# Optimization experiments

Hardware: AMD Instinct MI355X
Metric: run time of the kernel (lower is better)

Reference implementation:

```python
import jax, jax.numpy as jnp
import numpy as np

B, N, D, H = 64, 196, 768, 3072
QMAX = 127.0  # 8-bit symmetric: clamp to [-128, 127]


def ste_round(x):
    # straight-through-estimator round (QAT)
    return x + jax.lax.stop_gradient(jnp.round(x) - x)


def q_linear_diag(x, w, b, a_sf):
    """Quantized diagonal linear (ResMLP Affine / LayerScale as QuantLinear)."""
    w_sf = jnp.max(jnp.abs(w)) / QMAX            # per-tensor weight scale
    w_int = ste_round(w / w_sf)                  # int8 weights (|.|<=127)
    out_int = (x / a_sf) * w_int
    if b is not None:
        out_int = out_int + ste_round(b / (a_sf * w_sf))  # 32-bit bias
    return out_int * (a_sf * w_sf), w_sf


def q_linear_dense(x, w, b, a_sf):
    """Quantized dense linear: int8 GEMM + int32 bias, dequant with a_sf*w_sf."""
    w_sf = jnp.max(jnp.abs(w)) / QMAX
    w_int = jnp.clip(ste_round(w / w_sf), -QMAX - 1, QMAX)
    out_int = jnp.einsum('...i,oi->...o', x / a_sf, w_int) + ste_round(b / (a_sf * w_sf))
    return out_int * (a_sf * w_sf), w_sf


def q_act(x, pre_sf, new_sf, identity=None, id_sf=None):
    """HAWQ-style QuantAct: fixed-point requantization to scale new_sf (8-bit)."""
    if identity is None:
        z_int = ste_round(x / pre_sf)
        out_int = ste_round(z_int * (pre_sf / new_sf))
    else:
        # main branch (x - identity) requantized with pre_sf, identity with id_sf
        z_int = ste_round((x - identity) / pre_sf)
        out_int = ste_round(z_int * (pre_sf / new_sf)) \
                + ste_round(ste_round(identity / id_sf) * (id_sf / new_sf))
    out_int = jnp.clip(out_int, -QMAX - 1, QMAX)
    return out_int * new_sf, new_sf


def _forward(x, norm1_w, norm1_b, attn_w, attn_b, gamma1_w,
             norm2_w, norm2_b, fc1_w, fc1_b, fc2_w, fc2_b, gamma2_w, act_sfs):
    a_sf = act_sfs[0]
    # --- token-mixing half ---
    identity, id_sf = x, a_sf
    x, w_sf = q_linear_diag(x, norm1_w, norm1_b, a_sf)         # norm1 (affine)
    x = jnp.swapaxes(x, 1, 2)                                  # [B, D, N]
    x, a_sf = q_act(x, a_sf * w_sf, act_sfs[1])                # quant_act1
    x, w_sf = q_linear_dense(x, attn_w, attn_b, a_sf)          # attn (cross-patch)
    x = jnp.swapaxes(x, 1, 2)                                  # [B, N, D]
    x, a_sf = q_act(x, a_sf * w_sf, act_sfs[2])                # quant_act2
    x, w_sf = q_linear_diag(x, gamma1_w, None, a_sf)           # gamma_1 (layerscale)
    x = x + identity
    x, a_sf = q_act(x, a_sf * w_sf, act_sfs[3], identity, id_sf)  # quant_act_int32_1
    # --- MLP half ---
    identity, id_sf = x, a_sf
    x, w_sf = q_linear_diag(x, norm2_w, norm2_b, a_sf)         # norm2
    x, a_sf = q_act(x, a_sf * w_sf, act_sfs[4])                # quant_act3
    x, w_sf = q_linear_dense(x, fc1_w, fc1_b, a_sf)            # mlp.fc1
    x = jax.nn.relu(x)
    x, a_sf = q_act(x, a_sf * w_sf, act_sfs[5])                # mlp.quant_act1
    x, w_sf = q_linear_dense(x, fc2_w, fc2_b, a_sf)            # mlp.fc2
    x, a_sf = q_act(x, a_sf * w_sf, act_sfs[6])                # mlp.quant_act2
    x, w_sf = q_linear_diag(x, gamma2_w, None, a_sf)           # gamma_2
    x = x + identity
    x, a_sf = q_act(x, a_sf * w_sf, act_sfs[7], identity, id_sf)  # quant_act_int32_2
    return x, a_sf


def setup_inputs() -> dict:
    key = jax.random.key(0)
    ks = jax.random.split(key, 16)
    act_sfs = jax.random.uniform(ks[14], (8,), jnp.float32, 0.02, 0.06)
    x = jax.random.normal(ks[0], (B, N, D), jnp.float32)
    # input is already quantized at scale act_sfs[0]
    x = jnp.clip(jnp.round(x / act_sfs[0]), -128, 127) * act_sfs[0]
    s = 0.05
    return {
        'x': x,
        'norm1_w': 1.0 + s * jax.random.normal(ks[1], (D,), jnp.float32),
        'norm1_b': s * jax.random.normal(ks[2], (D,), jnp.float32),
        'attn_w': jax.random.normal(ks[3], (N, N), jnp.float32) / np.sqrt(N),
        'attn_b': s * jax.random.normal(ks[4], (N,), jnp.float32),
        'gamma1_w': 0.1 + s * jax.random.normal(ks[5], (D,), jnp.float32),
        'norm2_w': 1.0 + s * jax.random.normal(ks[6], (D,), jnp.float32),
        'norm2_b': s * jax.random.normal(ks[7], (D,), jnp.float32),
        'fc1_w': jax.random.normal(ks[8], (H, D), jnp.float32) / np.sqrt(D),
        'fc1_b': s * jax.random.normal(ks[9], (H,), jnp.float32),
        'fc2_w': jax.random.normal(ks[10], (D, H), jnp.float32) / np.sqrt(H),
        'fc2_b': s * jax.random.normal(ks[11], (D,), jnp.float32),
        'gamma2_w': 0.1 + s * jax.random.normal(ks[12], (D,), jnp.float32),
        'act_sfs': act_sfs,
    }


def reference(x, norm1_w, norm1_b, attn_w, attn_b, gamma1_w,
              norm2_w, norm2_b, fc1_w, fc1_b, fc2_w, fc2_b, gamma2_w, act_sfs):
    return _forward(x, norm1_w, norm1_b, attn_w, attn_b, gamma1_w,
                    norm2_w, norm2_b, fc1_w, fc1_b, fc2_w, fc2_b, gamma2_w, act_sfs)
```

## Files before the change

### kernel.cpp

```cpp
#include <hip/hip_runtime.h>

#define B_ 64
#define N_ 196
#define D_ 768
#define H_ 3072
#define M_ (B_*N_)
#define NP 256

typedef int int4v __attribute__((ext_vector_type(4)));
typedef signed char i8;

#define WS_MAX 0
#define WS_W1F 16
#define WS_B1F (16+768)
#define WS_G1F (16+768*2)
#define WS_W2F (16+768*3)
#define WS_B2F (16+768*4)
#define WS_G2F (16+768*5)
#define WS_BA  (16+768*6)
#define WS_BF1 (WS_BA+256)
#define WS_BF2 (WS_BF1+3072)
#define OFF_WA   40960ull
#define OFF_FC1  (OFF_WA+65536ull)
#define OFF_FC2  (OFF_FC1+2359296ull)
#define OFF_X2   (OFF_FC2+2359296ull)
#define OFF_Q3   (OFF_X2+9633792ull)
#define OFF_Q4   (OFF_Q3+9633792ull)
#define OFF_Q1T  OFF_Q4

__device__ __forceinline__ float clamp8(float v){ return fminf(fmaxf(v,-128.f),127.f); }

__device__ __forceinline__ void async16(const void* g, void* l){
    __builtin_amdgcn_global_load_lds((const __attribute__((address_space(1))) void*)g,
                                     (__attribute__((address_space(3))) void*)l, 16, 0, 0);
}

__global__ void k_init(char* ws, const float* __restrict__ act, float* out_tail){
    int id = blockIdx.x*256 + threadIdx.x;
    if (blockIdx.x == 0){
        float* f = (float*)ws;
        if (threadIdx.x < 8) f[WS_MAX+threadIdx.x] = 0.f;
        if (threadIdx.x == 8) *out_tail = act[7];
    }
    if (id < 4096){ int4v z = {0,0,0,0}; ((int4v*)(ws+OFF_WA))[id] = z; }
}

__global__ void k_maxabs(const float* __restrict__ p0, const float* __restrict__ p1,
                         const float* __restrict__ p2, const float* __restrict__ p3,
                         const float* __restrict__ p4, const float* __restrict__ p5,
                         const float* __restrict__ p6, float* wsmax){
    const float* ps[7] = {p0,p1,p2,p3,p4,p5,p6};
    const int    n4s[7] = {192, 9604, 192, 192, 589824, 589824, 192};
    int tid = blockIdx.y;
    const float4* p = (const float4*)ps[tid]; int n4 = n4s[tid];
    float m = 0.f;
    for (int i = blockIdx.x*blockDim.x + threadIdx.x; i < n4; i += gridDim.x*blockDim.x){
        float4 v = p[i];
        m = fmaxf(m, fmaxf(fmaxf(fabsf(v.x),fabsf(v.y)), fmaxf(fabsf(v.z),fabsf(v.w))));
    }
    #pragma unroll
    for (int off = 32; off; off >>= 1) m = fmaxf(m, __shfl_down(m, off, 64));
    __shared__ float red[4];
    int lane = threadIdx.x & 63, wv = threadIdx.x >> 6;
    if (lane == 0) red[wv] = m;
    __syncthreads();
    if (threadIdx.x == 0){
        float mm = red[0];
        for (int w = 1; w < (int)blockDim.x/64; w++) mm = fmaxf(mm, red[w]);
        atomicMax((unsigned*)&wsmax[tid], __float_as_uint(mm));
    }
}

__global__ void k_qweights(const float* __restrict__ n1w, const float* __restrict__ n1b,
                           const float* __restrict__ aw,  const float* __restrict__ ab,
                           const float* __restrict__ g1w, const float* __restrict__ n2w,
                           const float* __restrict__ n2b, const float* __restrict__ f1w,
                           const float* __restrict__ f1b, const float* __restrict__ f2w,
                           const float* __restrict__ f2b, const float* __restrict__ g2w,
                           const float* __restrict__ act, char* ws){
    float* fws = (float*)ws;
    int*   iws = (int*)ws;
    const float* mx = fws + WS_MAX;
    long i = (long)blockIdx.x*blockDim.x + threadIdx.x;
    const long F4 = 589824;
    if (i < F4){ float sf = mx[4]/127.0f;
        float4 v = ((const float4*)f1w)[i];
        char4 o = make_char4(
            (i8)(int)fminf(fmaxf(rintf(v.x/sf),-128.f),127.f),
            (i8)(int)fminf(fmaxf(rintf(v.y/sf),-128.f),127.f),
            (i8)(int)fminf(fmaxf(rintf(v.z/sf),-128.f),127.f),
            (i8)(int)fminf(fmaxf(rintf(v.w/sf),-128.f),127.f));
        ((char4*)(ws+OFF_FC1))[i] = o; return; }
    i -= F4;
    if (i < F4){ float sf = mx[5]/127.0f;
        float4 v = ((const float4*)f2w)[i];
        char4 o = make_char4(
            (i8)(int)fminf(fmaxf(rintf(v.x/sf),-128.f),127.f),
            (i8)(int)fminf(fmaxf(rintf(v.y/sf),-128.f),127.f),
            (i8)(int)fminf(fmaxf(rintf(v.z/sf),-128.f),127.f),
            (i8)(int)fminf(fmaxf(rintf(v.w/sf),-128.f),127.f));
        ((char4*)(ws+OFF_FC2))[i] = o; return; }
    i -= F4;
    if (i < 38416){ float sf = mx[1]/127.0f;
        int o = (int)(i/196), k = (int)(i%196);
        ((i8*)(ws+OFF_WA))[o*NP+k] = (i8)(int)fminf(fmaxf(rintf(aw[i]/sf),-128.f),127.f); return; }
    i -= 38416;
    if (i < 768){ float sf = mx[0]/127.0f; fws[WS_W1F+i] = rintf(n1w[i]/sf); return; }
    i -= 768;
    if (i < 768){ float sf = mx[0]/127.0f; fws[WS_B1F+i] = rintf(n1b[i]/(act[0]*sf)); return; }
    i -= 768;
    if (i < 768){ float sf = mx[2]/127.0f; fws[WS_G1F+i] = rintf(g1w[i]/sf); return; }
    i -= 768;
    if (i < 768){ float sf = mx[3]/127.0f; fws[WS_W2F+i] = rintf(n2w[i]/sf); return; }
    i -= 768;
    if (i < 768){ float sf = mx[3]/127.0f; fws[WS_B2F+i] = rintf(n2b[i]/(act[3]*sf)); return; }
    i -= 768;
    if (i < 768){ float sf = mx[6]/127.0f; fws[WS_G2F+i] = rintf(g2w[i]/sf); return; }
    i -= 768;
    if (i < 196){ float sf = mx[1]/127.0f; iws[WS_BA+i] = (int)rintf(ab[i]/(act[1]*sf)); return; }
    i -= 196;
    if (i < 3072){ float sf = mx[4]/127.0f; iws[WS_BF1+i] = (int)rintf(f1b[i]/(act[4]*sf)); return; }
    i -= 3072;
    if (i < 768){ float sf = mx[5]/127.0f; iws[WS_BF2+i] = (int)rintf(f2b[i]/(act[5]*sf)); return; }
}

__global__ __launch_bounds__(256) void k_stage1(const float* __restrict__ x,
                                                const char* __restrict__ wsc,
                                                char* __restrict__ ws,
                                                const float* __restrict__ act){
    __shared__ i8 T[64][68];
    const float* fws = (const float*)wsc;
    int b = blockIdx.z, n0 = blockIdx.y*64, d0 = blockIdx.x*64;
    int t = threadIdx.x;
    float a0 = act[0];
    float w1sf = fws[WS_MAX+0]/127.0f;
    float r1 = (a0*w1sf)/act[1];
    int dl = (t & 15) * 4;
    int d  = d0 + dl;
    float4 wv = *(const float4*)(fws + WS_W1F + d);
    float4 bv = *(const float4*)(fws + WS_B1F + d);
    #pragma unroll
    for (int pass = 0; pass < 4; pass++){
        int nl = (t >> 4) + pass*16;
        int n  = n0 + nl;
        i8 q[4] = {0,0,0,0};
        if (n < 196){
            float4 xv = *(const float4*)(x + ((size_t)b*196 + n)*768 + d);
            float o0 = rintf(xv.x/a0*wv.x + bv.x);
            float o1 = rintf(xv.y/a0*wv.y + bv.y);
            float o2 = rintf(xv.z/a0*wv.z + bv.z);
            float o3 = rintf(xv.w/a0*wv.w + bv.w);
            q[0] = (i8)(int)clamp8(rintf(o0*r1));
            q[1] = (i8)(int)clamp8(rintf(o1*r1));
            q[2] = (i8)(int)clamp8(rintf(o2*r1));
            q[3] = (i8)(int)clamp8(rintf(o3*r1));
        }
        T[dl+0][nl] = q[0]; T[dl+1][nl] = q[1];
        T[dl+2][nl] = q[2]; T[dl+3][nl] = q[3];
    }
    __syncthreads();
    i8* q1T = (i8*)(ws + OFF_Q1T) + (size_t)b*768*NP;
    #pragma unroll
    for (int e = 0; e < 4; e++){
        int id = t + e*256;
        int row = id >> 4, c = (id & 15) * 4;
        int v = *(const int*)&T[row][c];
        *(int*)(q1T + (size_t)(d0+row)*NP + n0 + c) = v;
    }
}

__device__ __forceinline__ void gemm_i8_dbuf(const i8* __restrict__ qa, const i8* __restrict__ wb,
                                             size_t lda, size_t ldb,
                                             int m0, int n0, int K, int4v acc[4][4],
                                             i8* As, i8* Bs, int t){
    int lane = t & 63;
    int w = t >> 6;
    int wm = w & 1, wn = w >> 1;
    int lr = lane >> 2, lc = lane & 3;
    const i8* ga = qa + (size_t)(m0 + w*32 + lr)*lda + lc*16;
    const i8* gb = wb + (size_t)(n0 + w*32 + lr)*ldb + lc*16;
    int loff = (w*32 + lr)*64 + lc*16;
    async16(ga,            As + loff);
    async16(ga + 16*lda,   As + loff + 16*64);
    async16(gb,            Bs + loff);
    async16(gb + 16*ldb,   Bs + loff + 16*64);
    int iters = K >> 6;
    for (int i = 0; i < iters; i++){
        __syncthreads();
        if (i+1 < iters){
            int kb = (i+1) << 6;
            int nb = ((i+1)&1) << 13;
            async16(ga + kb,            As + nb + loff);
            async16(ga + kb + 16*lda,   As + nb + loff + 16*64);
            async16(gb + kb,            Bs + nb + loff);
            async16(gb + kb + 16*ldb,   Bs + nb + loff + 16*64);
        }
        int cb = (i&1) << 13;
        int4v a[4], bb[4];
        #pragma unroll
        for (int mt = 0; mt < 4; mt++)
            a[mt] = *(const int4v*)(As + cb + (wm*64+mt*16+(lane&15))*64 + (lane>>4)*16);
        #pragma unroll
        for (int nt = 0; nt < 4; nt++)
            bb[nt] = *(const int4v*)(Bs + cb + (wn*64+nt*16+(lane&15))*64 + (lane>>4)*16);
        #pragma unroll
        for (int mt = 0; mt < 4; mt++)
            #pragma unroll
            for (int nt = 0; nt < 4; nt++)
                acc[mt][nt] = __builtin_amdgcn_mfma_i32_16x16x64_i8(a[mt], bb[nt], acc[mt][nt], 0,0,0);
    }
}

__global__ __launch_bounds__(256) void k_attn(const char* __restrict__ ws,
                                              const float* __restrict__ x,
                                              const float* __restrict__ act){
    __shared__ char smem[32768];
    const float* fws = (const float*)ws;
    const int*   iws = (const int*)ws;
    const i8* A  = (const i8*)(ws + OFF_WA);
    const i8* Bq = (const i8*)(ws + OFF_Q1T) + (size_t)blockIdx.z*768*NP;
    i8* x2 = (i8*)(ws + OFF_X2);
    i8* q3 = (i8*)(ws + OFF_Q3);
    int b = blockIdx.z;
    int m0 = blockIdx.x*128, n0 = blockIdx.y*128;
    int t = threadIdx.x, lane = t & 63;
    int wm = (t>>6)&1, wn = t>>7;
    int4v acc[4][4]; int4v zz = {0,0,0,0};
    #pragma unroll
    for (int mt=0;mt<4;mt++) for (int nt=0;nt<4;nt++) acc[mt][nt] = zz;
    gemm_i8_dbuf(A, Bq, NP, NP, m0, n0, NP, acc, (i8*)smem, (i8*)smem+16384, t);

    float a0=act[0], a1=act[1], a2=act[2], a3=act[3], a4=act[4];
    float wasf = fws[WS_MAX+1]/127.0f; float r2  = (a1*wasf)/a2;
    float g1sf = fws[WS_MAX+2]/127.0f; float r3a = (a2*g1sf)/a3; float r3b = a0/a3;
    float w2sf = fws[WS_MAX+3]/127.0f; float r4  = (a3*w2sf)/a4;
    float g1v[4], w2v[4], b2v[4];
    #pragma unroll
    for (int nt=0;nt<4;nt++){
        int d = n0 + wn*64 + nt*16 + (lane&15);
        g1v[nt] = fws[WS_G1F + d]; w2v[nt] = fws[WS_W2F + d]; b2v[nt] = fws[WS_B2F + d];
    }
    __syncthreads();
    i8* Xs = (i8*)smem;
    i8* Qs = (i8*)smem + 16384;
    #pragma unroll
    for (int mt=0;mt<4;mt++){
        #pragma unroll
        for (int r=0;r<4;r++){
            int ml = wm*64 + mt*16 + (lane>>4)*4 + r;
            int o  = m0 + ml;
            int ba = iws[WS_BA + o];
            #pragma unroll
            for (int nt=0;nt<4;nt++){
                int nl = wn*64 + nt*16 + (lane&15);
                int d  = n0 + nl;
                float s2 = (float)(acc[mt][nt][r] + ba);
                float q2 = clamp8(rintf(s2*r2));
                float o3v = q2*g1v[nt];
                float xv = (o < 196) ? x[((size_t)b*196 + o)*768 + d] : 0.f;
                float idi = rintf(xv/a0);
                float tt = rintf(o3v*r3a) + rintf(idi*r3b);
                tt = clamp8(tt);
                float o4 = tt*w2v[nt] + b2v[nt];
                float qr = clamp8(rintf(o4*r4));
                Xs[ml*128 + nl] = (i8)(int)tt;
                Qs[ml*128 + nl] = (i8)(int)qr;
            }
        }
    }
    __syncthreads();
    #pragma unroll
    for (int e=0;e<4;e++){
        int id = t + e*256;
        int row = id>>3, c = id&7;
        int o = m0 + row;
        if (o < 196){
            size_t g = ((size_t)b*196 + o)*768 + n0 + c*16;
            *(int4v*)(x2 + g) = *(const int4v*)(Xs + row*128 + c*16);
            *(int4v*)(q3 + g) = *(const int4v*)(Qs + row*128 + c*16);
        }
    }
}

__global__ __launch_bounds__(256) void k_fc1(const char* __restrict__ ws, const float* __restrict__ act){
    __shared__ char smem[32768];
    const float* fws = (const float*)ws;
    const int*   iws = (const int*)ws;
    const i8* qa = (const i8*)(ws+OFF_Q3);
    const i8* wb = (const i8*)(ws+OFF_FC1);
    const int* bias = iws + WS_BF1;
    i8* qout = (i8*)(ws+OFF_Q4);
    int m0 = blockIdx.x*128, n0 = blockIdx.y*128;
    int t = threadIdx.x, lane = t & 63;
    int wm = (t>>6)&1, wn = t>>7;
    int4v acc[4][4]; int4v zz = {0,0,0,0};
    #pragma unroll
    for (int mt=0;mt<4;mt++) for (int nt=0;nt<4;nt++) acc[mt][nt] = zz;
    gemm_i8_dbuf(qa, wb, 768, 768, m0, n0, 768, acc, (i8*)smem, (i8*)smem+16384, t);
    float wsf = fws[WS_MAX+4]/127.0f;
    float r5 = (act[4]*wsf)/act[5];
    int bcol[4];
    #pragma unroll
    for (int nt=0;nt<4;nt++) bcol[nt] = bias[n0 + wn*64 + nt*16 + (lane&15)];
    __syncthreads();
    i8* Cs = (i8*)smem;
    #pragma unroll
    for (int mt=0;mt<4;mt++){
        #pragma unroll
        for (int nt=0;nt<4;nt++){
            int nl = wn*64 + nt*16 + (lane&15);
            #pragma unroll
            for (int r=0;r<4;r++){
                int s = acc[mt][nt][r] + bcol[nt];
                if (s < 0) s = 0;
                float q = clamp8(rintf((float)s * r5));
                int ml = wm*64 + mt*16 + (lane>>4)*4 + r;
                Cs[ml*128 + nl] = (i8)(int)q;
            }
        }
    }
    __syncthreads();
    #pragma unroll
    for (int e=0;e<4;e++){
        int id2 = t + e*256;
        int row = id2>>3, c = id2&7;
        *(int4v*)(qout + (size_t)(m0+row)*3072 + n0 + c*16) = *(const int4v*)(Cs + row*128 + c*16);
    }
}

__global__ __launch_bounds__(256) void k_fc2(const char* __restrict__ ws, const float* __restrict__ act,
                                             float* __restrict__ out){
    __shared__ char smem[32768];
    const float* fws = (const float*)ws;
    const int*   iws = (const int*)ws;
    const i8* qa = (const i8*)(ws+OFF_Q4);
    const i8* wb = (const i8*)(ws+OFF_FC2);
    const int* bias = iws + WS_BF2;
    const float* g2f = fws + WS_G2F;
    const i8* x2 = (const i8*)(ws+OFF_X2);
    int m0 = blockIdx.x*128, n0 = blockIdx.y*128;
    int t = threadIdx.x, lane = t & 63;
    int wm = (t>>6)&1, wn = t>>7;
    int4v acc[4][4]; int4v zz = {0,0,0,0};
    #pragma unroll
    for (int mt=0;mt<4;mt++) for (int nt=0;nt<4;nt++) acc[mt][nt] = zz;
    gemm_i8_dbuf(qa, wb, 3072, 3072, m0, n0, 3072, acc, (i8*)smem, (i8*)smem+16384, t);
    float a3=act[3], a5=act[5], a6=act[6], a7=act[7];
    float wsf  = fws[WS_MAX+5]/127.0f; float r6  = (a5*wsf)/a6;
    float g2sf = fws[WS_MAX+6]/127.0f; float r7a = (a6*g2sf)/a7; float r7b = a3/a7;
    int bcol[4]; float g2v[4];
    #pragma unroll
    for (int nt=0;nt<4;nt++){
        int nc = n0 + wn*64 + nt*16 + (lane&15);
        bcol[nt] = bias[nc]; g2v[nt] = g2f[nc];
    }
    #pragma unroll
    for (int mt=0;mt<4;mt++){
        #pragma unroll
        for (int nt=0;nt<4;nt++){
            int nc = n0 + wn*64 + nt*16 + (lane&15);
            #pragma unroll
            for (int r=0;r<4;r++){
                int ml = wm*64 + mt*16 + (lane>>4)*4 + r;
                size_t gi = (size_t)(m0+ml)*768 + nc;
                int s = acc[mt][nt][r] + bcol[nt];
                float q6 = clamp8(rintf((float)s*r6));
                float o7 = q6*g2v[nt];
                float idi = (float)x2[gi];
                float tt = rintf(o7*r7a) + rintf(idi*r7b);
                tt = clamp8(tt);
                out[gi] = tt*a7;
            }
        }
    }
}

extern "C" void kernel_launch(void* const* d_in, const int* in_sizes, int n_in,
                              void* d_out, int out_size, void* d_ws, size_t ws_size,
                              hipStream_t stream){
    const float* x   = (const float*)d_in[0];
    const float* n1w = (const float*)d_in[1];
    const float* n1b = (const float*)d_in[2];
    const float* aw  = (const float*)d_in[3];
    const float* ab  = (const float*)d_in[4];
    const float* g1w = (const float*)d_in[5];
    const float* n2w = (const float*)d_in[6];
    const float* n2b = (const float*)d_in[7];
    const float* f1w = (const float*)d_in[8];
    const float* f1b = (const float*)d_in[9];
    const float* f2w = (const float*)d_in[10];
    const float* f2b = (const float*)d_in[11];
    const float* g2w = (const float*)d_in[12];
    const float* act = (const float*)d_in[13];
    char* ws = (char*)d_ws;
    float* out = (float*)d_out;

    k_init<<<16,256,0,stream>>>(ws, act, out + (size_t)B_*N_*D_);
    k_maxabs<<<dim3(120,7),256,0,stream>>>(n1w, aw, g1w, n2w, f1w, f2w, g2w, (float*)ws);
    long qwThreads = 2L*589824 + 38416 + 768L*6 + 196 + 3072 + 768;
    k_qweights<<<(int)((qwThreads+255)/256),256,0,stream>>>(n1w,n1b,aw,ab,g1w,n2w,n2b,
                                                            f1w,f1b,f2w,f2b,g2w,act,ws);
    k_stage1<<<dim3(12,4,64),256,0,stream>>>(x, ws, ws, act);
    k_attn<<<dim3(2,6,64),256,0,stream>>>(ws, x, act);
    k_fc1<<<dim3(98,24),256,0,stream>>>(ws, act);
    k_fc2<<<dim3(98,6),256,0,stream>>>(ws, act, out);
}
```

Baseline: 280.9 us.

## Use 512-thread blocks with 8 waves for fc1/fc2 int8 GEMMs

Splits each 128x128 output tile across 8 wavefronts (2x4 layout, 64x32 per wave) instead of 4, with a new GEMM helper where each thread issues one async 16-byte load per operand per K step. Per-wave accumulators halve, so register pressure drops and more waves are resident to hide latency. Each wave now rereads the A fragments with fewer MFMAs per load, so LDS traffic per MFMA rises and barriers cover more waves.

```diff
diff --git a/kernel.cpp b/kernel.cpp
--- a/kernel.cpp
+++ b/kernel.cpp
@@ -211,6 +211,46 @@
     }
 }
 
+__device__ __forceinline__ void gemm_i8_512(const i8* __restrict__ qa, const i8* __restrict__ wb,
+                                            size_t lda, size_t ldb,
+                                            int m0, int n0, int K, int4v acc[4][2],
+                                            i8* As, i8* Bs, int t){
+    int lane = t & 63;
+    int w = t >> 6;
+    int wm = w & 1, wn = w >> 1;
+    int sr = t >> 2, sc = t & 3;
+    const i8* ga = qa + (size_t)(m0 + sr)*lda + sc*16;
+    const i8* gb = wb + (size_t)(n0 + sr)*ldb + sc*16;
+    int loff = sr*64 + sc*16;
+    async16(ga, As + loff);
+    async16(gb, Bs + loff);
+    int arow = (wm*64 + (lane&15))*64 + (lane>>4)*16;
+    int brow = (wn*32 + (lane&15))*64 + (lane>>4)*16;
+    int iters = K >> 6;
+    for (int i = 0; i < iters; i++){
+        __syncthreads();
+        if (i+1 < iters){
+            int kb = (i+1) << 6;
+            int nb = ((i+1)&1) << 13;
+            async16(ga + kb, As + nb + loff);
+            async16(gb + kb, Bs + nb + loff);
+        }
+        int cb = (i&1) << 13;
+        int4v a[4], bb[2];
+        #pragma unroll
+        for (int mt = 0; mt < 4; mt++)
+            a[mt] = *(const int4v*)(As + cb + arow + mt*16*64);
+        #pragma unroll
+        for (int nt = 0; nt < 2; nt++)
+            bb[nt] = *(const int4v*)(Bs + cb + brow + nt*16*64);
+        #pragma unroll
+        for (int mt = 0; mt < 4; mt++)
+            #pragma unroll
+            for (int nt = 0; nt < 2; nt++)
+                acc[mt][nt] = __builtin_amdgcn_mfma_i32_16x16x64_i8(a[mt], bb[nt], acc[mt][nt], 0,0,0);
+    }
+}
+
 __global__ __launch_bounds__(256) void k_attn(const char* __restrict__ ws,
                                               const float* __restrict__ x,
                                               const float* __restrict__ act){
@@ -282,7 +322,7 @@
     }
 }
 
-__global__ __launch_bounds__(256) void k_fc1(const char* __restrict__ ws, const float* __restrict__ act){
+__global__ __launch_bounds__(512) void k_fc1(const char* __restrict__ ws, const float* __restrict__ act){
     __shared__ char smem[32768];
     const float* fws = (const float*)ws;
     const int*   iws = (const int*)ws;
@@ -292,23 +332,23 @@
     i8* qout = (i8*)(ws+OFF_Q4);
     int m0 = blockIdx.x*128, n0 = blockIdx.y*128;
     int t = threadIdx.x, lane = t & 63;
-    int wm = (t>>6)&1, wn = t>>7;
-    int4v acc[4][4]; int4v zz = {0,0,0,0};
-    #pragma unroll
-    for (int mt=0;mt<4;mt++) for (int nt=0;nt<4;nt++) acc[mt][nt] = zz;
-    gemm_i8_dbuf(qa, wb, 768, 768, m0, n0, 768, acc, (i8*)smem, (i8*)smem+16384, t);
+    int w = t >> 6, wm = w & 1, wn = w >> 1;
+    int4v acc[4][2]; int4v zz = {0,0,0,0};
+    #pragma unroll
+    for (int mt=0;mt<4;mt++) for (int nt=0;nt<2;nt++) acc[mt][nt] = zz;
+    gemm_i8_512(qa, wb, 768, 768, m0, n0, 768, acc, (i8*)smem, (i8*)smem+16384, t);
     float wsf = fws[WS_MAX+4]/127.0f;
     float r5 = (act[4]*wsf)/act[5];
-    int bcol[4];
-    #pragma unroll
-    for (int nt=0;nt<4;nt++) bcol[nt] = bias[n0 + wn*64 + nt*16 + (lane&15)];
+    int bcol[2];
+    #pragma unroll
+    for (int nt=0;nt<2;nt++) bcol[nt] = bias[n0 + wn*32 + nt*16 + (lane&15)];
     __syncthreads();
     i8* Cs = (i8*)smem;
     #pragma unroll
     for (int mt=0;mt<4;mt++){
         #pragma unroll
-        for (int nt=0;nt<4;nt++){
-            int nl = wn*64 + nt*16 + (lane&15);
+        for (int nt=0;nt<2;nt++){
+            int nl = wn*32 + nt*16 + (lane&15);
             #pragma unroll
             for (int r=0;r<4;r++){
                 int s = acc[mt][nt][r] + bcol[nt];
@@ -321,14 +361,14 @@
     }
     __syncthreads();
     #pragma unroll
-    for (int e=0;e<4;e++){
-        int id2 = t + e*256;
+    for (int e=0;e<2;e++){
+        int id2 = t + e*512;
         int row = id2>>3, c = id2&7;
         *(int4v*)(qout + (size_t)(m0+row)*3072 + n0 + c*16) = *(const int4v*)(Cs + row*128 + c*16);
     }
 }
 
-__global__ __launch_bounds__(256) void k_fc2(const char* __restrict__ ws, const float* __restrict__ act,
+__global__ __launch_bounds__(512) void k_fc2(const char* __restrict__ ws, const float* __restrict__ act,
                                              float* __restrict__ out){
     __shared__ char smem[32768];
     const float* fws = (const float*)ws;
@@ -340,25 +380,25 @@
     const i8* x2 = (const i8*)(ws+OFF_X2);
     int m0 = blockIdx.x*128, n0 = blockIdx.y*128;
     int t = threadIdx.x, lane = t & 63;
-    int wm = (t>>6)&1, wn = t>>7;
-    int4v acc[4][4]; int4v zz = {0,0,0,0};
-    #pragma unroll
-    for (int mt=0;mt<4;mt++) for (int nt=0;nt<4;nt++) acc[mt][nt] = zz;
-    gemm_i8_dbuf(qa, wb, 3072, 3072, m0, n0, 3072, acc, (i8*)smem, (i8*)smem+16384, t);
+    int w = t >> 6, wm = w & 1, wn = w >> 1;
+    int4v acc[4][2]; int4v zz = {0,0,0,0};
+    #pragma unroll
+    for (int mt=0;mt<4;mt++) for (int nt=0;nt<2;nt++) acc[mt][nt] = zz;
+    gemm_i8_512(qa, wb, 3072, 3072, m0, n0, 3072, acc, (i8*)smem, (i8*)smem+16384, t);
     float a3=act[3], a5=act[5], a6=act[6], a7=act[7];
     float wsf  = fws[WS_MAX+5]/127.0f; float r6  = (a5*wsf)/a6;
     float g2sf = fws[WS_MAX+6]/127.0f; float r7a = (a6*g2sf)/a7; float r7b = a3/a7;
-    int bcol[4]; float g2v[4];
-    #pragma unroll
-    for (int nt=0;nt<4;nt++){
-        int nc = n0 + wn*64 + nt*16 + (lane&15);
+    int bcol[2]; float g2v[2];
+    #pragma unroll
+    for (int nt=0;nt<2;nt++){
+        int nc = n0 + wn*32 + nt*16 + (lane&15);
         bcol[nt] = bias[nc]; g2v[nt] = g2f[nc];
     }
     #pragma unroll
     for (int mt=0;mt<4;mt++){
         #pragma unroll
-        for (int nt=0;nt<4;nt++){
-            int nc = n0 + wn*64 + nt*16 + (lane&15);
+        for (int nt=0;nt<2;nt++){
+            int nc = n0 + wn*32 + nt*16 + (lane&15);
             #pragma unroll
             for (int r=0;r<4;r++){
                 int ml = wm*64 + mt*16 + (lane>>4)*4 + r;
@@ -402,6 +442,6 @@
                                                             f1w,f1b,f2w,f2b,g2w,act,ws);
     k_stage1<<<dim3(12,4,64),256,0,stream>>>(x, ws, ws, act);
     k_attn<<<dim3(2,6,64),256,0,stream>>>(ws, x, act);
-    k_fc1<<<dim3(98,24),256,0,stream>>>(ws, act);
-    k_fc2<<<dim3(98,6),256,0,stream>>>(ws, act, out);
-}
+    k_fc1<<<dim3(98,24),512,0,stream>>>(ws, act);
+    k_fc2<<<dim3(98,6),512,0,stream>>>(ws, act, out);
+}
```

Measured after the change: 276.1 us. Within noise of the previous version (-1.7%).
